# Performance work log

Hardware: AMD Instinct MI355X
Metric: run time of the kernel (lower is better)

The kernel has to match this reference:

```python
import jax, jax.numpy as jnp
import numpy as np

EPS = 1e-5

def layernorm(x):
    mu = jnp.mean(x, axis=-1, keepdims=True)
    var = jnp.var(x, axis=-1, keepdims=True)
    return (x - mu) * jax.lax.rsqrt(var + EPS)

def jagged_to_padded(values, offsets, n):
    # values: [T, D]; offsets: [B+1]; -> [B, n, D] zero-padded
    lengths = offsets[1:] - offsets[:-1]            # [B]
    pos = jnp.arange(n)                             # [n]
    idx = offsets[:-1, None] + pos[None, :]         # [B, n]
    mask = pos[None, :] < lengths[:, None]          # [B, n]
    idx = jnp.clip(idx, 0, values.shape[0] - 1)
    return values[idx] * mask[..., None].astype(values.dtype)

def dense_to_jagged(padded, offsets, total):
    t = jnp.arange(total)
    b = jnp.searchsorted(offsets, t, side='right') - 1   # row of each token
    p = t - offsets[b]                                   # position within row
    return padded[b, p]

def causal_conv(x, w, b):
    # x: [B, n, D]; w: [D, D, 3]; residual + bias + leaky_relu
    xt = jnp.transpose(x, (0, 2, 1))                     # [B, D, n]
    xt = jnp.pad(xt, ((0, 0), (0, 0), (2, 0)))           # causal left pad (k-1)
    y = jax.lax.conv_general_dilated(xt, w, (1,), 'VALID',
                                     dimension_numbers=('NCH', 'OIH', 'NCH'))
    y = y + b[None, :, None]
    y = jnp.transpose(y, (0, 2, 1)) + x                  # residual
    return jax.nn.leaky_relu(y, 0.01)

def setup_inputs() -> dict:
    key = jax.random.key(0)
    ks = jax.random.split(key, 8)
    B, n, D = 32, 4096, 256
    P, H, dA = 512, 8, 64
    T = B * (n // 2)  # equal lengths of 2048
    offsets = (jnp.arange(B + 1, dtype=jnp.int64 if jax.config.read('jax_enable_x64') else jnp.int32) * (n // 2)).astype(jnp.int32)
    return {
        'normed_x': jax.random.normal(ks[0], (T, D), dtype=jnp.float32),
        'conv_w': 0.02 * jax.random.normal(ks[1], (D, D, 3), dtype=jnp.float32),
        'conv_b': 0.02 * jax.random.normal(ks[2], (D,), dtype=jnp.float32),
        'pattern': 0.02 * jax.random.normal(ks[3], (P, D), dtype=jnp.float32),
        'wq': 0.02 * jax.random.normal(ks[4], (H * dA, D), dtype=jnp.float32),
        'wkv': 0.02 * jax.random.normal(ks[5], (2 * H * dA, D), dtype=jnp.float32),
        'wout': jax.random.uniform(ks[6], (D, H * dA), dtype=jnp.float32,
                                   minval=-1.0, maxval=1.0) * np.sqrt(6.0 / (D + H * dA)),
        'bout': jnp.zeros((D,), dtype=jnp.float32),
        'x_offsets': offsets,
        'n': n,
    }

def reference(normed_x, conv_w, conv_b, pattern, wq, wkv, wout, bout, x_offsets, n):
    H, dA = 8, 64
    scale = dA ** (-0.5)
    T = normed_x.shape[0]
    # jagged -> padded, causal conv (residual + leaky_relu), padded -> jagged
    padded = jagged_to_padded(normed_x, x_offsets, n)        # [B, n, D]
    padded = causal_conv(padded, conv_w, conv_b)
    x = dense_to_jagged(padded, x_offsets, T)                # [T, D]
    # pattern layernormed twice (SPRM.forward then xattn.forward)
    pat = layernorm(layernorm(pattern))                      # [P, D]
    x = layernorm(x)
    q = (x @ wq.T).reshape(T, H, dA)                         # [T, H, dA]
    kv = (pat @ wkv.T).reshape(pat.shape[0], H, 2 * dA)
    k, v = kv[..., :dA], kv[..., dA:]                        # [P, H, dA]
    scores = scale * jnp.einsum('nhd,whd->nhw', q, k)        # [T, H, P]
    attn = jax.nn.softmax(scores, axis=-1)
    out = jnp.einsum('nhw,whd->nhd', attn, v).reshape(T, H * dA)
    out = out @ wout.T + bout                                # [T, D]
    return layernorm(out)
```

## Files before the change

kernel.cpp:

```cpp
#include <hip/hip_runtime.h>
#include <hip/hip_bf16.h>
#include <math.h>


#define EPSF 1e-5f

typedef short  s16x8 __attribute__((ext_vector_type(8)));
typedef short  s16x4 __attribute__((ext_vector_type(4)));
typedef float  f32x4 __attribute__((ext_vector_type(4)));

__device__ __forceinline__ unsigned short f2bf(float f) {
    union { float f; unsigned u; } v; v.f = f;
    unsigned r = (v.u + 0x7fffu + ((v.u >> 16) & 1u)) >> 16;
    return (unsigned short)r;
}
__device__ __forceinline__ float bf2f(unsigned short h) {
    union { unsigned u; float f; } v; v.u = ((unsigned)h) << 16;
    return v.f;
}
__device__ __forceinline__ unsigned fbits(float f) {
    union { float f; unsigned u; } v; v.f = f; return v.u;
}
__device__ __forceinline__ unsigned pk_hi(float lo, float hi) {
    return __builtin_amdgcn_perm(fbits(hi), fbits(lo), 0x07060302u);
}
__device__ __forceinline__ int inv32(int t) {
    return (t & ~31) | ((t & 0x0C) << 1) | ((t & 0x10) >> 2) | (t & 3);
}

union Bfrag { unsigned u[4]; s16x8 s; };

__global__ void cvt_kernel(const float* __restrict__ wq,
                           const float* __restrict__ wout,
                           const float* __restrict__ cw,
                           short* __restrict__ wq_bf,
                           short* __restrict__ wout_bf,
                           short* __restrict__ wck) {
    const int b = blockIdx.x, tid = threadIdx.x;
    if (b < 256) {
        const int i = ((b & 127) * 256 + tid) * 4;
        const float* src = (b < 128) ? wq : wout;
        short* dst = (b < 128) ? wq_bf : wout_bf;
        const float4 x = *(const float4*)(src + i);
        s16x4 o; o[0] = f2bf(x.x); o[1] = f2bf(x.y); o[2] = f2bf(x.z); o[3] = f2bf(x.w);
        *(s16x4*)(dst + i) = o;
    } else {
        const int idx = (b - 256) * 256 + tid;
        const float* p = cw + (size_t)idx * 3;
        wck[idx]              = (short)f2bf(p[0]);
        wck[65536 + idx]      = (short)f2bf(p[1]);
        wck[131072 + idx]     = (short)f2bf(p[2]);
    }
}

__global__ void pat_kv_kernel(const float* __restrict__ pattern,
                              const float* __restrict__ wkv,
                              short* __restrict__ k_bf,
                              short* __restrict__ v_t) {
    __shared__ __align__(16) float spat[256];
    __shared__ float scr[4];
    const int w = blockIdx.x;
    const int tid = threadIdx.x;
    const int lane = tid & 63, wav = tid >> 6;

    float v = pattern[(size_t)w * 256 + tid];

    float s = v;
    #pragma unroll
    for (int off = 32; off; off >>= 1) s += __shfl_xor(s, off);
    if (lane == 0) scr[wav] = s;
    __syncthreads();
    float mu = (scr[0] + scr[1] + scr[2] + scr[3]) * (1.f / 256.f);
    __syncthreads();
    float d = v - mu;
    float s2 = d * d;
    #pragma unroll
    for (int off = 32; off; off >>= 1) s2 += __shfl_xor(s2, off);
    if (lane == 0) scr[wav] = s2;
    __syncthreads();
    float var = (scr[0] + scr[1] + scr[2] + scr[3]) * (1.f / 256.f);
    float x1 = d * rsqrtf(var + EPSF);
    __syncthreads();

    s = x1;
    #pragma unroll
    for (int off = 32; off; off >>= 1) s += __shfl_xor(s, off);
    if (lane == 0) scr[wav] = s;
    __syncthreads();
    mu = (scr[0] + scr[1] + scr[2] + scr[3]) * (1.f / 256.f);
    __syncthreads();
    d = x1 - mu;
    s2 = d * d;
    #pragma unroll
    for (int off = 32; off; off >>= 1) s2 += __shfl_xor(s2, off);
    if (lane == 0) scr[wav] = s2;
    __syncthreads();
    var = (scr[0] + scr[1] + scr[2] + scr[3]) * (1.f / 256.f);
    float x2 = d * rsqrtf(var + EPSF);

    spat[tid] = x2;
    __syncthreads();

    #pragma unroll
    for (int u = 0; u < 4; u++) {
        const int j = tid + 256 * u;
        const float* wr = wkv + (size_t)j * 256;
        float acc = 0.f;
        for (int i4 = 0; i4 < 64; i4++) {
            float4 w4 = *(const float4*)(wr + i4 * 4);
            float4 x4 = *(const float4*)(&spat[i4 * 4]);
            acc += w4.x * x4.x + w4.y * x4.y + w4.z * x4.z + w4.w * x4.w;
        }
        const int h = j >> 7, r = j & 127;
        if (r < 64)
            k_bf[((size_t)h * 512 + w) * 64 + inv32(r)] = (short)f2bf(acc);
        else
            v_t[(size_t)h * 32768 + (size_t)(r - 64) * 512 + inv32(w)] = (short)f2bf(acc);
    }
}

__global__ __launch_bounds__(256, 4)
void conv_ln_kernel(const float* __restrict__ x,
                    const short* __restrict__ wck,
                    const float* __restrict__ cb,
                    short* __restrict__ xn_bf) {
    __shared__ __align__(16) short xs[66 * 268];
    const int tid = threadIdx.x;
    const int r0 = blockIdx.x * 64;
    const int pos0 = r0 & 2047;

    #pragma unroll
    for (int it = 0; it < 17; it++) {
        const int idx = tid + it * 256;
        if (idx < 4224) {
            const int row = idx >> 6, c4 = idx & 63;
            float4 v = {0.f, 0.f, 0.f, 0.f};
            if (pos0 - 2 + row >= 0)
                v = *(const float4*)(x + (size_t)(r0 - 2 + row) * 256 + c4 * 4);
            s16x4 o; o[0] = f2bf(v.x); o[1] = f2bf(v.y); o[2] = f2bf(v.z); o[3] = f2bf(v.w);
            *(s16x4*)(xs + row * 268 + c4 * 4) = o;
        }
    }
    __syncthreads();

    const int lane = tid & 63, w = tid >> 6, g = lane >> 4, cl = lane & 15;

    f32x4 acc[4][4];
    #pragma unroll
    for (int mt = 0; mt < 4; mt++)
        #pragma unroll
        for (int nt = 0; nt < 4; nt++) acc[mt][nt] = (f32x4){0.f, 0.f, 0.f, 0.f};

    #pragma unroll
    for (int kk = 0; kk < 3; kk++) {
        const short* wb = wck + kk * 65536;
        for (int s = 0; s < 8; s++) {
            s16x8 a[4];
            #pragma unroll
            for (int mt = 0; mt < 4; mt++)
                a[mt] = *(const s16x8*)(xs + (mt * 16 + cl + kk) * 268 + s * 32 + g * 8);
            #pragma unroll
            for (int nt = 0; nt < 4; nt++) {
                const s16x8 b = *(const s16x8*)(wb + (size_t)(w * 64 + nt * 16 + cl) * 256 + s * 32 + g * 8);
                #pragma unroll
                for (int mt = 0; mt < 4; mt++)
                    acc[mt][nt] = __builtin_amdgcn_mfma_f32_16x16x32_bf16(a[mt], b, acc[mt][nt], 0, 0, 0);
            }
        }
    }

    #pragma unroll
    for (int nt = 0; nt < 4; nt++) {
        const int col = w * 64 + nt * 16 + cl;
        const float b = cb[col];
        #pragma unroll
        for (int mt = 0; mt < 4; mt++)
            #pragma unroll
            for (int r = 0; r < 4; r++) {
                const int row = mt * 16 + g * 4 + r;
                float y = acc[mt][nt][r] + b + x[(size_t)(r0 + row) * 256 + col];
                acc[mt][nt][r] = (y >= 0.f) ? y : 0.01f * y;
            }
    }
    __syncthreads();
    #pragma unroll
    for (int mt = 0; mt < 4; mt++)
        #pragma unroll
        for (int nt = 0; nt < 4; nt++)
            #pragma unroll
            for (int r = 0; r < 4; r++)
                xs[(mt * 16 + g * 4 + r) * 268 + w * 64 + nt * 16 + cl] =
                    (short)f2bf(acc[mt][nt][r]);
    __syncthreads();

    for (int q = 0; q < 16; q++) {
        const int m = w * 16 + q;
        const s16x4 v4 = *(const s16x4*)(xs + m * 268 + lane * 4);
        const float f0 = bf2f((unsigned short)v4[0]), f1 = bf2f((unsigned short)v4[1]);
        const float f2 = bf2f((unsigned short)v4[2]), f3 = bf2f((unsigned short)v4[3]);
        float s = f0 + f1 + f2 + f3;
        #pragma unroll
        for (int off = 32; off; off >>= 1) s += __shfl_xor(s, off);
        const float mu = s * (1.f / 256.f);
        const float d0 = f0 - mu, d1 = f1 - mu, d2 = f2 - mu, d3 = f3 - mu;
        float vv = d0 * d0 + d1 * d1 + d2 * d2 + d3 * d3;
        #pragma unroll
        for (int off = 32; off; off >>= 1) vv += __shfl_xor(vv, off);
        const float rs = rsqrtf(vv * (1.f / 256.f) + EPSF);
        s16x4 o; o[0] = f2bf(d0 * rs); o[1] = f2bf(d1 * rs);
        o[2] = f2bf(d2 * rs); o[3] = f2bf(d3 * rs);
        *(s16x4*)(xn_bf + (size_t)(r0 + m) * 256 + lane * 4) = o;
    }
}

__global__ __launch_bounds__(256, 3)
void qattn_kernel(const short* __restrict__ xn_bf,
                  const short* __restrict__ wq_bf,
                  const short* __restrict__ k_bf,
                  const short* __restrict__ v_t,
                  short* __restrict__ ao_bf) {
    __shared__ __align__(16) unsigned char smem[35840];
    short* k_s = (short*)smem;
    short* v_s = (short*)(smem + 18432);

    const int tid = threadIdx.x;
    const int lane = tid & 63, w = tid >> 6, g = lane >> 4, cl = lane & 15;
    const int r0 = blockIdx.x * 64;
    const int q_row = r0 + w * 16 + cl;

    for (int h = 0; h < 8; ++h) {
        f32x4 qacc[4];
        #pragma unroll
        for (int nt = 0; nt < 4; nt++) qacc[nt] = (f32x4){0.f, 0.f, 0.f, 0.f};
        for (int s = 0; s < 8; ++s) {
            const s16x8 bx = *(const s16x8*)(xn_bf + (size_t)q_row * 256 + s * 32 + g * 8);
            #pragma unroll
            for (int nt = 0; nt < 4; ++nt) {
                const s16x8 aw = *(const s16x8*)(wq_bf + (size_t)(h * 64 + nt * 16 + cl) * 256 + s * 32 + g * 8);
                qacc[nt] = __builtin_amdgcn_mfma_f32_16x16x32_bf16(aw, bx, qacc[nt], 0, 0, 0);
            }
        }
        Bfrag qB[2];
        #pragma unroll
        for (int s = 0; s < 2; ++s) {
            qB[s].u[0] = pk_hi(qacc[2 * s][0],     qacc[2 * s][1]);
            qB[s].u[1] = pk_hi(qacc[2 * s][2],     qacc[2 * s][3]);
            qB[s].u[2] = pk_hi(qacc[2 * s + 1][0], qacc[2 * s + 1][1]);
            qB[s].u[3] = pk_hi(qacc[2 * s + 1][2], qacc[2 * s + 1][3]);
        }

        float lsum = 0.f;
        f32x4 oacc[4];
        #pragma unroll
        for (int nd = 0; nd < 4; nd++) oacc[nd] = (f32x4){0.f, 0.f, 0.f, 0.f};

        for (int ck = 0; ck < 4; ++ck) {
            __syncthreads();
            {
                const uint4* gk = (const uint4*)(k_bf + ((size_t)(h * 512 + ck * 128 + (tid >> 1)) * 64 + (tid & 1) * 32));
                uint4* lk = (uint4*)((char*)k_s + (tid >> 1) * 144 + (tid & 1) * 64);
                uint4 d0 = gk[0], d1 = gk[1], d2 = gk[2], d3 = gk[3];
                lk[0] = d0; lk[1] = d1; lk[2] = d2; lk[3] = d3;
                const uint4* gv = (const uint4*)(v_t + (size_t)h * 32768 + (size_t)(tid >> 2) * 512 + ck * 128 + (tid & 3) * 32);
                uint4* lv = (uint4*)((char*)v_s + (tid >> 2) * 272 + (tid & 3) * 64);
                uint4 e0 = gv[0], e1 = gv[1], e2 = gv[2], e3 = gv[3];
                lv[0] = e0; lv[1] = e1; lv[2] = e2; lv[3] = e3;
            }
            __syncthreads();

            f32x4 sa[8];
            #pragma unroll
            for (int nt = 0; nt < 8; nt++) sa[nt] = (f32x4){0.f, 0.f, 0.f, 0.f};
            #pragma unroll
            for (int nt = 0; nt < 8; nt++) {
                const char* kb = (const char*)k_s + (nt * 16 + cl) * 144 + g * 16;
                sa[nt] = __builtin_amdgcn_mfma_f32_16x16x32_bf16(*(const s16x8*)kb,        qB[0].s, sa[nt], 0, 0, 0);
                sa[nt] = __builtin_amdgcn_mfma_f32_16x16x32_bf16(*(const s16x8*)(kb + 64), qB[1].s, sa[nt], 0, 0, 0);
            }

            #pragma unroll
            for (int nt = 0; nt < 8; nt++)
                #pragma unroll
                for (int r = 0; r < 4; r++) {
                    const float p = __expf(0.125f * sa[nt][r]);
                    lsum += p;
                    sa[nt][r] = p;
                }

            #pragma unroll
            for (int ks = 0; ks < 4; ++ks) {
                Bfrag pB;
                pB.u[0] = pk_hi(sa[2 * ks][0],     sa[2 * ks][1]);
                pB.u[1] = pk_hi(sa[2 * ks][2],     sa[2 * ks][3]);
                pB.u[2] = pk_hi(sa[2 * ks + 1][0], sa[2 * ks + 1][1]);
                pB.u[3] = pk_hi(sa[2 * ks + 1][2], sa[2 * ks + 1][3]);
                #pragma unroll
                for (int nd = 0; nd < 4; ++nd) {
                    const char* vb = (const char*)v_s + (nd * 16 + cl) * 272 + ks * 64 + g * 16;
                    oacc[nd] = __builtin_amdgcn_mfma_f32_16x16x32_bf16(*(const s16x8*)vb, pB.s, oacc[nd], 0, 0, 0);
                }
            }
        }

        lsum += __shfl_xor(lsum, 16);
        lsum += __shfl_xor(lsum, 32);
        const float inv = 1.f / lsum;
        #pragma unroll
        for (int nd = 0; nd < 4; ++nd)
            #pragma unroll
            for (int r = 0; r < 4; ++r)
                ao_bf[(size_t)q_row * 512 + h * 64 + nd * 16 + 4 * g + r] =
                    (short)f2bf(oacc[nd][r] * inv);
    }
}

__global__ __launch_bounds__(256, 4)
void outproj_ln_kernel(const short* __restrict__ ao,
                       const short* __restrict__ wout_bf,
                       const float* __restrict__ bout,
                       float* __restrict__ out) {
    __shared__ __align__(16) char smem[33280];
    short* as = (short*)smem;
    float* ys = (float*)smem;
    const int tid = threadIdx.x;
    const int r0 = blockIdx.x * 32;

    #pragma unroll
    for (int it = 0; it < 8; it++) {
        const int idx = tid + it * 256;
        const int row = idx >> 6, c8 = idx & 63;
        const s16x8 v = *(const s16x8*)(ao + (size_t)(r0 + row) * 512 + c8 * 8);
        *(s16x8*)(as + row * 520 + c8 * 8) = v;
    }
    __syncthreads();

    const int lane = tid & 63, w = tid >> 6, g = lane >> 4, cl = lane & 15;

    f32x4 acc[2][4];
    #pragma unroll
    for (int mt = 0; mt < 2; mt++)
        #pragma unroll
        for (int nt = 0; nt < 4; nt++) acc[mt][nt] = (f32x4){0.f, 0.f, 0.f, 0.f};

    for (int s = 0; s < 16; s++) {
        const s16x8 a0 = *(const s16x8*)(as + cl * 520 + s * 32 + g * 8);
        const s16x8 a1 = *(const s16x8*)(as + (16 + cl) * 520 + s * 32 + g * 8);
        #pragma unroll
        for (int nt = 0; nt < 4; nt++) {
            const s16x8 b = *(const s16x8*)(wout_bf + (size_t)(w * 64 + nt * 16 + cl) * 512 + s * 32 + g * 8);
            acc[0][nt] = __builtin_amdgcn_mfma_f32_16x16x32_bf16(a0, b, acc[0][nt], 0, 0, 0);
            acc[1][nt] = __builtin_amdgcn_mfma_f32_16x16x32_bf16(a1, b, acc[1][nt], 0, 0, 0);
        }
    }
    __syncthreads();

    #pragma unroll
    for (int nt = 0; nt < 4; nt++) {
        const int col = w * 64 + nt * 16 + cl;
        const float b = bout[col];
        #pragma unroll
        for (int mt = 0; mt < 2; mt++)
            #pragma unroll
            for (int r = 0; r < 4; r++)
                ys[(mt * 16 + g * 4 + r) * 260 + col] = acc[mt][nt][r] + b;
    }
    __syncthreads();

    for (int q = 0; q < 8; q++) {
        const int m = w * 8 + q;
        const float4 v4 = *(const float4*)(ys + m * 260 + lane * 4);
        float s = v4.x + v4.y + v4.z + v4.w;
        #pragma unroll
        for (int off = 32; off; off >>= 1) s += __shfl_xor(s, off);
        const float mu = s * (1.f / 256.f);
        const float d0 = v4.x - mu, d1 = v4.y - mu, d2 = v4.z - mu, d3 = v4.w - mu;
        float vv = d0 * d0 + d1 * d1 + d2 * d2 + d3 * d3;
        #pragma unroll
        for (int off = 32; off; off >>= 1) vv += __shfl_xor(vv, off);
        const float rs = rsqrtf(vv * (1.f / 256.f) + EPSF);
        float4 o; o.x = d0 * rs; o.y = d1 * rs; o.z = d2 * rs; o.w = d3 * rs;
        *(float4*)(out + (size_t)(r0 + m) * 256 + lane * 4) = o;
    }
}

extern "C" void kernel_launch(void* const* d_in, const int* in_sizes, int n_in,
                              void* d_out, int out_size, void* d_ws, size_t ws_size,
                              hipStream_t stream) {
    const float* normed_x = (const float*)d_in[0];
    const float* conv_w   = (const float*)d_in[1];
    const float* conv_b   = (const float*)d_in[2];
    const float* pattern  = (const float*)d_in[3];
    const float* wq       = (const float*)d_in[4];
    const float* wkv      = (const float*)d_in[5];
    const float* wout     = (const float*)d_in[6];
    const float* bout     = (const float*)d_in[7];
    const int T = in_sizes[0] / 256;

    char* wsb = (char*)d_ws;
    short* xn_bf  = (short*)(wsb);
    short* ao_bf  = (short*)(wsb + (size_t)33554432);
    short* k_bf   = (short*)(wsb + (size_t)100663296);
    short* v_t    = (short*)(wsb + (size_t)101187584);
    short* wq_bf  = (short*)(wsb + (size_t)101711872);
    short* wout_bf= (short*)(wsb + (size_t)101974016);
    short* wck    = (short*)(wsb + (size_t)102236160);
    float* out    = (float*)d_out;

    cvt_kernel<<<512, 256, 0, stream>>>(wq, wout, conv_w, wq_bf, wout_bf, wck);
    pat_kv_kernel<<<512, 256, 0, stream>>>(pattern, wkv, k_bf, v_t);
    conv_ln_kernel<<<T / 64, 256, 0, stream>>>(normed_x, wck, conv_b, xn_bf);
    qattn_kernel<<<T / 64, 256, 0, stream>>>(xn_bf, wq_bf, k_bf, v_t, ao_bf);
    outproj_ln_kernel<<<T / 32, 256, 0, stream>>>(ao_bf, wout_bf, bout, out);
}
```

Baseline: 540.1 us.

## Double-buffer swizzled K/V via async LDS loads and double rows per wave

```diff
diff --git a/kernel.cpp b/kernel.cpp
--- a/kernel.cpp
+++ b/kernel.cpp
@@ -8,6 +8,13 @@
 typedef short  s16x8 __attribute__((ext_vector_type(8)));
 typedef short  s16x4 __attribute__((ext_vector_type(4)));
 typedef float  f32x4 __attribute__((ext_vector_type(4)));
+
+typedef __attribute__((address_space(3))) unsigned int       lds_u32_t;
+typedef __attribute__((address_space(1))) const unsigned int glb_u32_t;
+
+__device__ __forceinline__ void gload_lds16(const void* g, void* l) {
+    __builtin_amdgcn_global_load_lds((glb_u32_t*)g, (lds_u32_t*)l, 16, 0, 0);
+}
 
 __device__ __forceinline__ unsigned short f2bf(float f) {
     union { float f; unsigned u; } v; v.f = f;
@@ -112,10 +119,20 @@
             acc += w4.x * x4.x + w4.y * x4.y + w4.z * x4.z + w4.w * x4.w;
         }
         const int h = j >> 7, r = j & 127;
-        if (r < 64)
-            k_bf[((size_t)h * 512 + w) * 64 + inv32(r)] = (short)f2bf(acc);
-        else
-            v_t[(size_t)h * 32768 + (size_t)(r - 64) * 512 + inv32(w)] = (short)f2bf(acc);
+        if (r < 64) {
+            const int c = inv32(r);
+            const int ck = w >> 7, crow = w & 127;
+            const int un = c >> 3, ph = un ^ (crow & 7);
+            k_bf[(size_t)h * 32768 + ck * 8192 + crow * 64 + ph * 8 + (c & 7)]
+                = (short)f2bf(acc * 0.125f);
+        } else {
+            const int rd = r - 64;
+            const int c = inv32(w);
+            const int ck = c >> 7, cc = c & 127;
+            const int un = cc >> 3, ph = un ^ (rd & 15);
+            v_t[(size_t)h * 32768 + ck * 8192 + rd * 128 + ph * 8 + (cc & 7)]
+                = (short)f2bf(acc);
+        }
     }
 }
 
@@ -213,104 +230,145 @@
     }
 }
 
-__global__ __launch_bounds__(256, 3)
+__global__ __launch_bounds__(256, 2)
 void qattn_kernel(const short* __restrict__ xn_bf,
                   const short* __restrict__ wq_bf,
                   const short* __restrict__ k_bf,
                   const short* __restrict__ v_t,
                   short* __restrict__ ao_bf) {
-    __shared__ __align__(16) unsigned char smem[35840];
-    short* k_s = (short*)smem;
-    short* v_s = (short*)(smem + 18432);
+    __shared__ __align__(16) char smem[65536];
 
     const int tid = threadIdx.x;
     const int lane = tid & 63, w = tid >> 6, g = lane >> 4, cl = lane & 15;
-    const int r0 = blockIdx.x * 64;
-    const int q_row = r0 + w * 16 + cl;
+    const int r0 = blockIdx.x * 128;
+    const int q0 = r0 + w * 32 + cl;
+
+    const char* kv_base = (w < 2) ? (const char*)k_bf : (const char*)v_t;
+    const int   half    = (w & 1) * 8192;
+
+    {
+        const char* src = kv_base + half + lane * 16;
+        char* dst = smem + w * 8192;
+        #pragma unroll
+        for (int i = 0; i < 8; i++)
+            gload_lds16(src + i * 1024, dst + i * 1024);
+    }
 
     for (int h = 0; h < 8; ++h) {
-        f32x4 qacc[4];
-        #pragma unroll
-        for (int nt = 0; nt < 4; nt++) qacc[nt] = (f32x4){0.f, 0.f, 0.f, 0.f};
+        f32x4 qacc[2][4];
+        #pragma unroll
+        for (int u = 0; u < 2; u++)
+            #pragma unroll
+            for (int nt = 0; nt < 4; nt++) qacc[u][nt] = (f32x4){0.f, 0.f, 0.f, 0.f};
         for (int s = 0; s < 8; ++s) {
-            const s16x8 bx = *(const s16x8*)(xn_bf + (size_t)q_row * 256 + s * 32 + g * 8);
+            const s16x8 bx0 = *(const s16x8*)(xn_bf + (size_t)q0 * 256 + s * 32 + g * 8);
+            const s16x8 bx1 = *(const s16x8*)(xn_bf + ((size_t)q0 + 16) * 256 + s * 32 + g * 8);
             #pragma unroll
             for (int nt = 0; nt < 4; ++nt) {
                 const s16x8 aw = *(const s16x8*)(wq_bf + (size_t)(h * 64 + nt * 16 + cl) * 256 + s * 32 + g * 8);
-                qacc[nt] = __builtin_amdgcn_mfma_f32_16x16x32_bf16(aw, bx, qacc[nt], 0, 0, 0);
-            }
-        }
-        Bfrag qB[2];
-        #pragma unroll
-        for (int s = 0; s < 2; ++s) {
-            qB[s].u[0] = pk_hi(qacc[2 * s][0],     qacc[2 * s][1]);
-            qB[s].u[1] = pk_hi(qacc[2 * s][2],     qacc[2 * s][3]);
-            qB[s].u[2] = pk_hi(qacc[2 * s + 1][0], qacc[2 * s + 1][1]);
-            qB[s].u[3] = pk_hi(qacc[2 * s + 1][2], qacc[2 * s + 1][3]);
-        }
-
-        float lsum = 0.f;
-        f32x4 oacc[4];
-        #pragma unroll
-        for (int nd = 0; nd < 4; nd++) oacc[nd] = (f32x4){0.f, 0.f, 0.f, 0.f};
+                qacc[0][nt] = __builtin_amdgcn_mfma_f32_16x16x32_bf16(aw, bx0, qacc[0][nt], 0, 0, 0);
+                qacc[1][nt] = __builtin_amdgcn_mfma_f32_16x16x32_bf16(aw, bx1, qacc[1][nt], 0, 0, 0);
+            }
+        }
+        Bfrag qB[2][2];
+        #pragma unroll
+        for (int u = 0; u < 2; ++u)
+            #pragma unroll
+            for (int s = 0; s < 2; ++s) {
+                qB[u][s].u[0] = pk_hi(qacc[u][2 * s][0],     qacc[u][2 * s][1]);
+                qB[u][s].u[1] = pk_hi(qacc[u][2 * s][2],     qacc[u][2 * s][3]);
+                qB[u][s].u[2] = pk_hi(qacc[u][2 * s + 1][0], qacc[u][2 * s + 1][1]);
+                qB[u][s].u[3] = pk_hi(qacc[u][2 * s + 1][2], qacc[u][2 * s + 1][3]);
+            }
+
+        float lsum[2] = {0.f, 0.f};
+        f32x4 oacc[2][4];
+        #pragma unroll
+        for (int u = 0; u < 2; u++)
+            #pragma unroll
+            for (int nd = 0; nd < 4; nd++) oacc[u][nd] = (f32x4){0.f, 0.f, 0.f, 0.f};
 
         for (int ck = 0; ck < 4; ++ck) {
+            const int step = h * 4 + ck;
+            const int buf = step & 1;
             __syncthreads();
-            {
-                const uint4* gk = (const uint4*)(k_bf + ((size_t)(h * 512 + ck * 128 + (tid >> 1)) * 64 + (tid & 1) * 32));
-                uint4* lk = (uint4*)((char*)k_s + (tid >> 1) * 144 + (tid & 1) * 64);
-                uint4 d0 = gk[0], d1 = gk[1], d2 = gk[2], d3 = gk[3];
-                lk[0] = d0; lk[1] = d1; lk[2] = d2; lk[3] = d3;
-                const uint4* gv = (const uint4*)(v_t + (size_t)h * 32768 + (size_t)(tid >> 2) * 512 + ck * 128 + (tid & 3) * 32);
-                uint4* lv = (uint4*)((char*)v_s + (tid >> 2) * 272 + (tid & 3) * 64);
-                uint4 e0 = gv[0], e1 = gv[1], e2 = gv[2], e3 = gv[3];
-                lv[0] = e0; lv[1] = e1; lv[2] = e2; lv[3] = e3;
-            }
-            __syncthreads();
-
-            f32x4 sa[8];
-            #pragma unroll
-            for (int nt = 0; nt < 8; nt++) sa[nt] = (f32x4){0.f, 0.f, 0.f, 0.f};
+            if (step + 1 < 32) {
+                const int ns = step + 1;
+                const char* src = kv_base + (size_t)(ns >> 2) * 65536
+                                + (ns & 3) * 16384 + half + lane * 16;
+                char* dst = smem + (buf ^ 1) * 32768 + w * 8192;
+                #pragma unroll
+                for (int i = 0; i < 8; i++)
+                    gload_lds16(src + i * 1024, dst + i * 1024);
+            }
+            const char* kc = smem + buf * 32768;
+            const char* vc = kc + 16384;
+
+            f32x4 sa[2][8];
+            #pragma unroll
+            for (int u = 0; u < 2; u++)
+                #pragma unroll
+                for (int nt = 0; nt < 8; nt++) sa[u][nt] = (f32x4){0.f, 0.f, 0.f, 0.f};
             #pragma unroll
             for (int nt = 0; nt < 8; nt++) {
-                const char* kb = (const char*)k_s + (nt * 16 + cl) * 144 + g * 16;
-                sa[nt] = __builtin_amdgcn_mfma_f32_16x16x32_bf16(*(const s16x8*)kb,        qB[0].s, sa[nt], 0, 0, 0);
-                sa[nt] = __builtin_amdgcn_mfma_f32_16x16x32_bf16(*(const s16x8*)(kb + 64), qB[1].s, sa[nt], 0, 0, 0);
-            }
-
-            #pragma unroll
-            for (int nt = 0; nt < 8; nt++)
-                #pragma unroll
-                for (int r = 0; r < 4; r++) {
-                    const float p = __expf(0.125f * sa[nt][r]);
-                    lsum += p;
-                    sa[nt][r] = p;
+                const char* kb = kc + ((nt * 16 + cl) << 7);
+                const s16x8 a0 = *(const s16x8*)(kb + ((g       ^ (cl & 7)) << 4));
+                const s16x8 a1 = *(const s16x8*)(kb + (((4 + g) ^ (cl & 7)) << 4));
+                sa[0][nt] = __builtin_amdgcn_mfma_f32_16x16x32_bf16(a0, qB[0][0].s, sa[0][nt], 0, 0, 0);
+                sa[0][nt] = __builtin_amdgcn_mfma_f32_16x16x32_bf16(a1, qB[0][1].s, sa[0][nt], 0, 0, 0);
+                sa[1][nt] = __builtin_amdgcn_mfma_f32_16x16x32_bf16(a0, qB[1][0].s, sa[1][nt], 0, 0, 0);
+                sa[1][nt] = __builtin_amdgcn_mfma_f32_16x16x32_bf16(a1, qB[1][1].s, sa[1][nt], 0, 0, 0);
+            }
+
+            #pragma unroll
+            for (int u = 0; u < 2; u++)
+                #pragma unroll
+                for (int nt = 0; nt < 8; nt++)
+                    #pragma unroll
+                    for (int r = 0; r < 4; r++) {
+                        const float p = __expf(sa[u][nt][r]);
+                        lsum[u] += p;
+                        sa[u][nt][r] = p;
+                    }
+
+            #pragma unroll
+            for (int ks = 0; ks < 4; ++ks) {
+                Bfrag pB[2];
+                #pragma unroll
+                for (int u = 0; u < 2; u++) {
+                    pB[u].u[0] = pk_hi(sa[u][2 * ks][0],     sa[u][2 * ks][1]);
+                    pB[u].u[1] = pk_hi(sa[u][2 * ks][2],     sa[u][2 * ks][3]);
+                    pB[u].u[2] = pk_hi(sa[u][2 * ks + 1][0], sa[u][2 * ks + 1][1]);
+                    pB[u].u[3] = pk_hi(sa[u][2 * ks + 1][2], sa[u][2 * ks + 1][3]);
                 }
-
-            #pragma unroll
-            for (int ks = 0; ks < 4; ++ks) {
-                Bfrag pB;
-                pB.u[0] = pk_hi(sa[2 * ks][0],     sa[2 * ks][1]);
-                pB.u[1] = pk_hi(sa[2 * ks][2],     sa[2 * ks][3]);
-                pB.u[2] = pk_hi(sa[2 * ks + 1][0], sa[2 * ks + 1][1]);
-                pB.u[3] = pk_hi(sa[2 * ks + 1][2], sa[2 * ks + 1][3]);
                 #pragma unroll
                 for (int nd = 0; nd < 4; ++nd) {
-                    const char* vb = (const char*)v_s + (nd * 16 + cl) * 272 + ks * 64 + g * 16;
-                    oacc[nd] = __builtin_amdgcn_mfma_f32_16x16x32_bf16(*(const s16x8*)vb, pB.s, oacc[nd], 0, 0, 0);
+                    const char* vb = vc + ((nd * 16 + cl) << 8) + (((ks * 4 + g) ^ cl) << 4);
+                    const s16x8 av = *(const s16x8*)vb;
+                    oacc[0][nd] = __builtin_amdgcn_mfma_f32_16x16x32_bf16(av, pB[0].s, oacc[0][nd], 0, 0, 0);
+                    oacc[1][nd] = __builtin_amdgcn_mfma_f32_16x16x32_bf16(av, pB[1].s, oacc[1][nd], 0, 0, 0);
                 }
             }
         }
 
-        lsum += __shfl_xor(lsum, 16);
-        lsum += __shfl_xor(lsum, 32);
-        const float inv = 1.f / lsum;
-        #pragma unroll
-        for (int nd = 0; nd < 4; ++nd)
-            #pragma unroll
-            for (int r = 0; r < 4; ++r)
-                ao_bf[(size_t)q_row * 512 + h * 64 + nd * 16 + 4 * g + r] =
-                    (short)f2bf(oacc[nd][r] * inv);
+        #pragma unroll
+        for (int u = 0; u < 2; ++u) {
+            float s = lsum[u];
+            s += __shfl_xor(s, 16);
+            s += __shfl_xor(s, 32);
+            const float inv = 1.f / s;
+            const size_t qr = (size_t)(q0 + u * 16);
+            #pragma unroll
+            for (int nd = 0; nd < 4; ++nd) {
+                const float o0 = oacc[u][nd][0] * inv, o1 = oacc[u][nd][1] * inv;
+                const float o2 = oacc[u][nd][2] * inv, o3 = oacc[u][nd][3] * inv;
+                const unsigned lo = (unsigned)f2bf(o0) | ((unsigned)f2bf(o1) << 16);
+                const unsigned hi = (unsigned)f2bf(o2) | ((unsigned)f2bf(o3) << 16);
+                short* dst = ao_bf + qr * 512 + h * 64 + nd * 16 + 4 * g;
+                *(unsigned*)(dst)     = lo;
+                *(unsigned*)(dst + 2) = hi;
+            }
+        }
     }
 }
 
@@ -409,6 +467,6 @@
     cvt_kernel<<<512, 256, 0, stream>>>(wq, wout, conv_w, wq_bf, wout_bf, wck);
     pat_kv_kernel<<<512, 256, 0, stream>>>(pattern, wkv, k_bf, v_t);
     conv_ln_kernel<<<T / 64, 256, 0, stream>>>(normed_x, wck, conv_b, xn_bf);
-    qattn_kernel<<<T / 64, 256, 0, stream>>>(xn_bf, wq_bf, k_bf, v_t, ao_bf);
+    qattn_kernel<<<T / 128, 256, 0, stream>>>(xn_bf, wq_bf, k_bf, v_t, ao_bf);
     outproj_ln_kernel<<<T / 32, 256, 0, stream>>>(ao_bf, wout_bf, bout, out);
 }
```

Result: slower. 563.0 us (+4.2%).
